# Kernel optimization log

Hardware: AMD Instinct MI355X
Metric: run time of the kernel (lower is better)

The kernel has to match this reference:

```python
import math
import jax, jax.numpy as jnp
import numpy as np

B_, L_, D_, N_, R_ = 4, 1024, 1024, 16, 64  # batch, seq, n_embd(=dim_inner), d_state, dt_rank


def setup_inputs() -> dict:
    key = jax.random.key(0)
    ks = jax.random.split(key, 6)
    s = lambda k, shp: jax.random.normal(k, shp, jnp.float32) * 0.02
    return {
        "x": jax.random.normal(ks[0], (B_, L_, D_), jnp.float32),
        "ln1_w": jnp.ones((D_,), jnp.float32),
        "ln2_w": jnp.ones((D_,), jnp.float32),
        "W_dbc": s(ks[1], (R_ + 2 * N_, D_)),   # x -> [delta_lowrank, B, C]
        "W_dt": s(ks[2], (D_, R_)),              # dt_rank -> dim_inner
        "b_dt": jnp.zeros((D_,), jnp.float32),
        "A_log": jnp.log(jnp.broadcast_to(jnp.arange(1, N_ + 1, dtype=jnp.float32), (D_, N_))),
        "Dp": jnp.ones((D_,), jnp.float32),      # skip-connection D parameter
        "W_fc": s(ks[3], (4 * D_, D_)),
        "W_proj": s(ks[4], (D_, 4 * D_)),
    }


def _layernorm(x, w):
    mu = jnp.mean(x, -1, keepdims=True)
    xc = x - mu
    var = jnp.mean(xc * xc, -1, keepdims=True)
    return xc * jax.lax.rsqrt(var + 1e-5) * w


def _new_gelu(x):
    c = math.sqrt(2.0 / math.pi)
    return 0.5 * x * (1.0 + jnp.tanh(c * (x + 0.044715 * x * x * x)))


def _ssm(x, W_dbc, W_dt, b_dt, A_log, Dp):
    # x: (b, l, d) with d == dim_inner == n_embd
    dbc = jnp.einsum("bld,ed->ble", x, W_dbc)                # (b,l,R+2N)
    delta, Bm, Cm = jnp.split(dbc, [R_, R_ + N_], axis=-1)
    delta = jax.nn.softplus(jnp.einsum("blr,dr->bld", delta, W_dt) + b_dt)  # (b,l,d)
    A = -jnp.exp(A_log)                                       # (d,n)
    dA = jnp.exp(delta[..., None] * A)                        # (b,l,d,n) discretized A
    dBx = (delta * x)[..., None] * Bm[:, :, None, :]          # (b,l,d,n) discretized B*x

    # h_t = dA_t * h_{t-1} + dBx_t  -> parallel first-order linear scan
    def combine(e1, e2):
        a1, b1 = e1
        a2, b2 = e2
        return a2 * a1, a2 * b1 + b2

    _, hs = jax.lax.associative_scan(combine, (dA, dBx), axis=1)
    y = jnp.einsum("bldn,bln->bld", hs, Cm)
    return y + x * Dp


def reference(x, ln1_w, ln2_w, W_dbc, W_dt, b_dt, A_log, Dp, W_fc, W_proj):
    h = jax.nn.softplus(_layernorm(x, ln1_w))
    h = h + _ssm(h, W_dbc, W_dt, b_dt, A_log, Dp)
    m = _layernorm(h, ln2_w)
    m = _new_gelu(jnp.einsum("bld,fd->blf", m, W_fc))
    m = jnp.einsum("blf,df->bld", m, W_proj)
    return h + m
```

## Files before the change

### kernel.cpp

```cpp
#include <hip/hip_runtime.h>
#include <cstdint>
#include <cstddef>

typedef unsigned short u16;
typedef unsigned int u32;
typedef __attribute__((ext_vector_type(8))) short short8;
typedef __attribute__((ext_vector_type(4))) float floatx4;
typedef __attribute__((ext_vector_type(4))) u16 u16x4;

#define DEV static __device__ __forceinline__

DEV u16 f2b(float f){ u32 u = __float_as_uint(f); u32 r = u + 0x7fffu + ((u>>16)&1u); return (u16)(r>>16); }
DEV float softplusf(float z){ return fmaxf(z,0.f) + log1pf(__expf(-fabsf(z))); }
DEV float fast_tanhf(float u){ float e = __expf(2.f*u); return 1.f - 2.f/(e+1.f); }
DEV float geluf(float x){ float u = 0.7978845608028654f*(x + 0.044715f*x*x*x); return 0.5f*x*(1.f+fast_tanhf(u)); }

DEV void async_copy16(const void* gp, void* lp){
  __builtin_amdgcn_global_load_lds((const __attribute__((address_space(1))) u32*)gp,
                                   (__attribute__((address_space(3))) u32*)lp, 16, 0, 0);
}

__global__ __launch_bounds__(256)
void prep_weights(const float* __restrict__ Wdbc, const float* __restrict__ Wdt,
                  const float* __restrict__ Wfc, const float* __restrict__ Wproj,
                  u16* __restrict__ dbc_b, u16* __restrict__ dt_b,
                  u16* __restrict__ fc_b, u16* __restrict__ pj_b)
{
  int i = blockIdx.x*256 + threadIdx.x;
  const float* src; u16* dst; int j;
  if (i < 32768){
    int e = i*4, r = e >> 10;
    if (r >= 96){ u16x4 z = {0,0,0,0}; *(u16x4*)(dbc_b + e) = z; return; }
    src = Wdbc; dst = dbc_b; j = i;
  } else if (i < 49152){ src = Wdt;   dst = dt_b; j = i - 32768; }
  else if (i < 1097728){ src = Wfc;   dst = fc_b; j = i - 49152; }
  else                 { src = Wproj; dst = pj_b; j = i - 1097728; }
  float4 v = ((const float4*)src)[j];
  u16x4 o = { f2b(v.x), f2b(v.y), f2b(v.z), f2b(v.w) };
  *(u16x4*)(dst + j*4) = o;
}

__global__ void dbc_post(const float* __restrict__ p, u16* __restrict__ delta_in,
                         float* __restrict__ BCf){
  int e = blockIdx.x*256 + threadIdx.x;
  int t = e >> 7, c = e & 127;
  float s = 0.f;
  #pragma unroll
  for (int z=0;z<8;z++) s += p[(size_t)z*524288 + e];
  if (c < 64)      delta_in[t*64 + c] = f2b(s);
  else if (c < 96) BCf[t*32 + (c-64)] = s;
}

__global__ void proj_reduce(const float* __restrict__ p, const float* __restrict__ h1f,
                            float* __restrict__ out){
  int i = blockIdx.x*256 + threadIdx.x;
  float4 a = ((const float4*)p)[i];
  float4 b = ((const float4*)(p + (size_t) 4194304))[i];
  float4 c = ((const float4*)(p + (size_t) 8388608))[i];
  float4 d = ((const float4*)(p + (size_t)12582912))[i];
  float4 r = ((const float4*)h1f)[i];
  float4 o = make_float4(a.x+b.x+c.x+d.x+r.x, a.y+b.y+c.y+d.y+r.y,
                         a.z+b.z+c.z+d.z+r.z, a.w+b.w+c.w+d.w+r.w);
  ((float4*)out)[i] = o;
}

__global__ __launch_bounds__(256)
void ln1_kernel(const float* __restrict__ x, const float* __restrict__ w,
                float* __restrict__ h0f, u16* __restrict__ h0b)
{
  int row = blockIdx.x, tid = threadIdx.x;
  const float4* xr = (const float4*)(x + (size_t)row*1024);
  float4 v = xr[tid];
  float s1 = v.x+v.y+v.z+v.w;
  float s2 = v.x*v.x+v.y*v.y+v.z*v.z+v.w*v.w;
  #pragma unroll
  for (int m=1;m<64;m<<=1){ s1 += __shfl_xor(s1,m); s2 += __shfl_xor(s2,m); }
  __shared__ float red[8];
  int wv = tid>>6;
  if ((tid&63)==0){ red[wv]=s1; red[4+wv]=s2; }
  __syncthreads();
  s1 = red[0]+red[1]+red[2]+red[3];
  s2 = red[4]+red[5]+red[6]+red[7];
  float mu  = s1*(1.f/1024.f);
  float var = s2*(1.f/1024.f) - mu*mu;
  float rstd = rsqrtf(var + 1e-5f);
  float4 wv4 = ((const float4*)w)[tid];
  float o0 = softplusf((v.x-mu)*rstd*wv4.x);
  float o1 = softplusf((v.y-mu)*rstd*wv4.y);
  float o2 = softplusf((v.z-mu)*rstd*wv4.z);
  float o3 = softplusf((v.w-mu)*rstd*wv4.w);
  ((float4*)(h0f + (size_t)row*1024))[tid] = make_float4(o0,o1,o2,o3);
  u16x4 ob = { f2b(o0), f2b(o1), f2b(o2), f2b(o3) };
  *(u16x4*)(h0b + (size_t)row*1024 + tid*4) = ob;
}

__global__ __launch_bounds__(256)
void ln2_kernel(const float* __restrict__ x, const float* __restrict__ w,
                u16* __restrict__ outb)
{
  int row = blockIdx.x, tid = threadIdx.x;
  const float4* xr = (const float4*)(x + (size_t)row*1024);
  float4 v = xr[tid];
  float s1 = v.x+v.y+v.z+v.w;
  float s2 = v.x*v.x+v.y*v.y+v.z*v.z+v.w*v.w;
  #pragma unroll
  for (int m=1;m<64;m<<=1){ s1 += __shfl_xor(s1,m); s2 += __shfl_xor(s2,m); }
  __shared__ float red[8];
  int wv = tid>>6;
  if ((tid&63)==0){ red[wv]=s1; red[4+wv]=s2; }
  __syncthreads();
  s1 = red[0]+red[1]+red[2]+red[3];
  s2 = red[4]+red[5]+red[6]+red[7];
  float mu  = s1*(1.f/1024.f);
  float var = s2*(1.f/1024.f) - mu*mu;
  float rstd = rsqrtf(var + 1e-5f);
  float4 wv4 = ((const float4*)w)[tid];
  u16x4 ob = { f2b((v.x-mu)*rstd*wv4.x), f2b((v.y-mu)*rstd*wv4.y),
               f2b((v.z-mu)*rstd*wv4.z), f2b((v.w-mu)*rstd*wv4.w) };
  *(u16x4*)(outb + (size_t)row*1024 + tid*4) = ob;
}

template<int EPI, int SWZ>
__global__ __launch_bounds__(256)
void gemm_bt(const u16* __restrict__ A, int lda,
             const u16* __restrict__ B, int ldb, int K,
             float* __restrict__ outF, u16* __restrict__ outB, int ldo,
             const float* __restrict__ bias, size_t zstr)
{
  __shared__ u16 sA[128*32];
  __shared__ u16 sB[128*32];
  const int tid = threadIdx.x;
  int m_blk, n_blk, zb;
  if (SWZ == 0){ n_blk = blockIdx.x; m_blk = blockIdx.y; zb = blockIdx.z; }
  else if (SWZ == 1){
    int b = blockIdx.x, xcd = b & 7, local = b >> 3;
    m_blk = (xcd>>2)*16 + (local & 15);
    n_blk = (xcd&3)*8 + (local >> 4);
    zb = 0;
  } else {
    int b = blockIdx.x, xcd = b & 7, local = b >> 3;
    m_blk = (xcd>>1)*8 + (local & 7);
    n_blk = local >> 3;
    zb = xcd & 1;
  }
  const int m0 = m_blk*128, n0 = n_blk*128;
  const int kstart = zb * K;
  const int wave = tid>>6, lane = tid&63;
  const int wm = (wave>>1)*64, wn = (wave&1)*64;
  const int lr = lane&15, quad = lane>>4;

  floatx4 acc[4][4];
  #pragma unroll
  for (int i=0;i<4;i++)
    #pragma unroll
    for (int j=0;j<4;j++){ floatx4 z = {0.f,0.f,0.f,0.f}; acc[i][j]=z; }

  const int r0 = tid>>2;
  const int kc8 = (((tid&3) ^ ((tid>>3)&3)))*8;
  const int sswz = ((lr>>1)&3);
  for (int k0=kstart; k0<kstart+K; k0+=32){
    __syncthreads();
    async_copy16(A + (size_t)(m0+r0)*lda    + k0+kc8, &sA[(size_t)tid*8]);
    async_copy16(A + (size_t)(m0+64+r0)*lda + k0+kc8, &sA[(size_t)(tid+256)*8]);
    async_copy16(B + (size_t)(n0+r0)*ldb    + k0+kc8, &sB[(size_t)tid*8]);
    async_copy16(B + (size_t)(n0+64+r0)*ldb + k0+kc8, &sB[(size_t)(tid+256)*8]);
    __syncthreads();
    short8 af[4], bf[4];
    #pragma unroll
    for (int i=0;i<4;i++){
      af[i] = *(const short8*)&sA[(wm+i*16+lr)*32 + (quad^sswz)*8];
      bf[i] = *(const short8*)&sB[(wn+i*16+lr)*32 + (quad^sswz)*8];
    }
    #pragma unroll
    for (int i=0;i<4;i++)
      #pragma unroll
      for (int j=0;j<4;j++)
        acc[i][j] = __builtin_amdgcn_mfma_f32_16x16x32_bf16(af[i], bf[j], acc[i][j], 0,0,0);
  }
  #pragma unroll
  for (int i=0;i<4;i++){
    #pragma unroll
    for (int j=0;j<4;j++){
      #pragma unroll
      for (int r=0;r<4;r++){
        int gr = m0 + wm + i*16 + quad*4 + r;
        int gc = n0 + wn + j*16 + lr;
        float v = acc[i][j][r];
        size_t o = (size_t)gr*ldo + gc;
        if (EPI==1)      outF[o] = softplusf(v + bias[gc]);
        else if (EPI==2) outB[o] = f2b(geluf(v));
        else             outF[zstr*zb + o] = v;
      }
    }
  }
}

template<int EPI, int SWZ>
__global__ __launch_bounds__(512, 2)
void gemm256(const u16* __restrict__ A, int lda,
             const u16* __restrict__ B, int ldb, int K,
             float* __restrict__ outF, u16* __restrict__ outB, int ldo,
             size_t zstr)
{
  __shared__ u16 sA[2][4][4096];
  __shared__ u16 sB[2][4][4096];
  const int tid = threadIdx.x;
  int m_blk, n_blk, zb;
  if (SWZ == 3){
    int b = blockIdx.x, xcd = b & 7, local = b >> 3;
    m_blk = (xcd>>2)*8 + (local & 7);
    n_blk = (xcd&3)*4 + (local >> 3);
    zb = 0;
  } else {
    int b = blockIdx.x, xcd = b & 7, local = b >> 3;
    zb    = xcd >> 1;
    m_blk = (xcd&1)*8 + (local & 7);
    n_blk = local >> 3;
  }
  const int m0 = m_blk*256, n0 = n_blk*256;
  const int kstart = zb*K;
  const int wave = tid>>6, lane = tid&63;
  const int mq = wave>>2, nq = wave&3;
  const int lr = lane&15, quad = lane>>4;
  const int sswz = (lr>>1)&3;

  const int srow = tid>>2;
  const int scol = ((tid&3) ^ ((tid>>3)&3))*8;
  const u16* pa = A + (size_t)(m0 + srow)*lda + scol;
  const u16* pb = B + (size_t)(n0 + srow)*ldb + scol;
  u16* la = (u16*)sA + tid*8;
  u16* lb = (u16*)sB + tid*8;
  const size_t ah128 = (size_t)128*lda;
  const size_t bh128 = (size_t)128*ldb;

  const int a_rd = (mq*64 + lr)*32 + (quad^sswz)*8;
  const int b_rd = ((nq&1)*64 + lr)*32 + (quad^sswz)*8;
  const int bun  = nq>>1;

  floatx4 acc[2][4][4];
  #pragma unroll
  for (int h=0;h<2;h++)
    #pragma unroll
    for (int i=0;i<4;i++)
      #pragma unroll
      for (int j=0;j<4;j++){ floatx4 z={0.f,0.f,0.f,0.f}; acc[h][i][j]=z; }

#define STG_A(NB,KS,H,KT) async_copy16(pa + (size_t)(H)*ah128 + (size_t)((KT) + (KS)*32), \
                                       la + (NB)*16384 + ((KS)*2+(H))*4096)
#define STG_B(NB,KS,H,KT) async_copy16(pb + (size_t)(H)*bh128 + (size_t)((KT) + (KS)*32), \
                                       lb + (NB)*16384 + ((KS)*2+(H))*4096)

#define PHASE(CUR, KA, AH, VM, ...)                                           \
  {                                                                           \
    asm volatile("s_waitcnt vmcnt(" VM ")" ::: "memory");                     \
    asm volatile("s_barrier" ::: "memory");                                   \
    __VA_ARGS__;                                                              \
    const u16* ca = (const u16*)sA + (CUR)*16384 + ((KA)*2+(AH))*4096;        \
    const u16* cb = (const u16*)sB + (CUR)*16384 + ((KA)*2+bun)*4096;         \
    short8 af[4], bf[4];                                                      \
    _Pragma("unroll")                                                         \
    for (int i_=0;i_<4;i_++){                                                 \
      af[i_] = *(const short8*)(ca + a_rd + i_*512);                          \
      bf[i_] = *(const short8*)(cb + b_rd + i_*512);                          \
    }                                                                         \
    __builtin_amdgcn_s_setprio(1);                                            \
    _Pragma("unroll")                                                         \
    for (int i_=0;i_<4;i_++)                                                  \
      _Pragma("unroll")                                                       \
      for (int j_=0;j_<4;j_++)                                                \
        acc[AH][i_][j_] = __builtin_amdgcn_mfma_f32_16x16x32_bf16(            \
            af[i_], bf[j_], acc[AH][i_][j_], 0,0,0);                          \
    __builtin_amdgcn_s_setprio(0);                                            \
  }

  STG_A(0,0,0,kstart); STG_B(0,0,0,kstart);
  STG_B(0,0,1,kstart); STG_A(0,0,1,kstart);
  STG_B(0,1,0,kstart); STG_B(0,1,1,kstart);
  STG_A(0,1,0,kstart); STG_A(0,1,1,kstart);

  const int NT = K >> 6;
  int cur = 0;
  int ktn = kstart + 64;
  for (int t=0; t<NT-1; ++t, ktn += 64, cur ^= 1){
    const int nb = cur^1;
    PHASE(cur, 0,0, "5", STG_A(nb,0,0,ktn); STG_B(nb,0,0,ktn));
    PHASE(cur, 0,1, "6", STG_B(nb,0,1,ktn); STG_A(nb,0,1,ktn));
    PHASE(cur, 1,0, "5", STG_B(nb,1,0,ktn); STG_B(nb,1,1,ktn));
    PHASE(cur, 1,1, "6", STG_A(nb,1,0,ktn); STG_A(nb,1,1,ktn));
  }
  PHASE(cur, 0,0, "5", );
  PHASE(cur, 0,1, "4", );
  PHASE(cur, 1,0, "1", );
  PHASE(cur, 1,1, "0", );

#undef PHASE
#undef STG_A
#undef STG_B

  #pragma unroll
  for (int h=0;h<2;h++){
    #pragma unroll
    for (int i=0;i<4;i++){
      #pragma unroll
      for (int j=0;j<4;j++){
        #pragma unroll
        for (int r=0;r<4;r++){
          int gr = m0 + h*128 + mq*64 + i*16 + quad*4 + r;
          int gc = n0 + nq*64 + j*16 + lr;
          float v = acc[h][i][j][r];
          size_t o = (size_t)gr*ldo + gc;
          if (EPI==2) outB[o] = f2b(geluf(v));
          else        outF[zstr*zb + o] = v;
        }
      }
    }
  }
}

__global__ __launch_bounds__(256)
void scan_p1(const float* __restrict__ delta, const float* __restrict__ h0f,
             const float* __restrict__ BCf, const float* __restrict__ A_log,
             float* __restrict__ Pbuf, float* __restrict__ Sbuf)
{
  int blk = blockIdx.x;
  int d = (blk & 3)*256 + threadIdx.x;
  int c = (blk >> 2) & 31;
  int b = blk >> 7;
  float a2[16], h[16], P[16];
  #pragma unroll
  for (int n=0;n<16;n++){ a2[n] = -__expf(A_log[d*16+n]) * 1.44269504f; h[n]=0.f; P[n]=1.f; }
  int t0 = c*32;
  const float* dptr = delta + ((size_t)(b*1024 + t0))*1024 + d;
  const float* xptr = h0f   + ((size_t)(b*1024 + t0))*1024 + d;
  const float* bc   = BCf   + ((size_t)(b*1024 + t0))*32;
  #pragma unroll 4
  for (int t=0;t<32;t++){
    float dlt = dptr[t*1024];
    float xv  = xptr[t*1024];
    float dx = dlt*xv;
    #pragma unroll
    for (int n=0;n<16;n++){
      float dA = exp2f(dlt*a2[n]);
      h[n] = dA*h[n] + dx*bc[t*32+n];
      P[n] *= dA;
    }
  }
  size_t base = ((size_t)((b*32 + c)*16))*1024 + d;
  #pragma unroll
  for (int n=0;n<16;n++){ Pbuf[base + (size_t)n*1024] = P[n]; Sbuf[base + (size_t)n*1024] = h[n]; }
}

__global__ __launch_bounds__(256)
void scan_p2(const float* __restrict__ Pbuf, const float* __restrict__ Sbuf,
             float* __restrict__ Hbuf)
{
  int blk = blockIdx.x;
  int d = (blk & 3)*256 + threadIdx.x;
  int n = (blk >> 2) & 15;
  int b = blk >> 6;
  float H = 0.f;
  for (int c=0;c<32;c++){
    size_t idx = ((size_t)((b*32 + c)*16 + n))*1024 + d;
    float P = Pbuf[idx], S = Sbuf[idx];
    Hbuf[idx] = H;
    H = P*H + S;
  }
}

__global__ __launch_bounds__(256)
void scan_p3(const float* __restrict__ delta, const float* __restrict__ h0f,
             const float* __restrict__ BCf, const float* __restrict__ A_log,
             const float* __restrict__ Hbuf, const float* __restrict__ Dp,
             float* __restrict__ h1f)
{
  int blk = blockIdx.x;
  int d = (blk & 3)*256 + threadIdx.x;
  int c = (blk >> 2) & 31;
  int b = blk >> 7;
  float a2[16], h[16];
  size_t hb = ((size_t)((b*32 + c)*16))*1024 + d;
  #pragma unroll
  for (int n=0;n<16;n++){
    a2[n] = -__expf(A_log[d*16+n]) * 1.44269504f;
    h[n] = Hbuf[hb + (size_t)n*1024];
  }
  float dpv = 1.f + Dp[d];
  int t0 = c*32;
  const float* dptr = delta + ((size_t)(b*1024 + t0))*1024 + d;
  const float* xptr = h0f   + ((size_t)(b*1024 + t0))*1024 + d;
  const float* bc   = BCf   + ((size_t)(b*1024 + t0))*32;
  float* optr = h1f + ((size_t)(b*1024 + t0))*1024 + d;
  #pragma unroll 4
  for (int t=0;t<32;t++){
    float dlt = dptr[t*1024];
    float xv  = xptr[t*1024];
    float dx = dlt*xv;
    float y = 0.f;
    #pragma unroll
    for (int n=0;n<16;n++){
      float dA = exp2f(dlt*a2[n]);
      h[n] = dA*h[n] + dx*bc[t*32+n];
      y += h[n]*bc[t*32+16+n];
    }
    optr[t*1024] = xv*dpv + y;
  }
}

extern "C" void kernel_launch(void* const* d_in, const int* in_sizes, int n_in,
                              void* d_out, int out_size, void* d_ws, size_t ws_size,
                              hipStream_t stream)
{
  const float* x    = (const float*)d_in[0];
  const float* ln1w = (const float*)d_in[1];
  const float* ln2w = (const float*)d_in[2];
  const float* Wdbc = (const float*)d_in[3];
  const float* Wdt  = (const float*)d_in[4];
  const float* bdt  = (const float*)d_in[5];
  const float* Alog = (const float*)d_in[6];
  const float* Dp   = (const float*)d_in[7];
  const float* Wfc  = (const float*)d_in[8];
  const float* Wproj= (const float*)d_in[9];
  float* out = (float*)d_out;

  char* ws = (char*)d_ws;
  size_t off = 0;
  auto carve = [&](size_t bytes)->char*{ char* p = ws + off; off += (bytes + 255) & ~(size_t)255; return p; };
  const size_t T = 4096;
  float* h0f   = (float*)carve(T*1024*4);
  float* h1f   = (float*)carve(T*1024*4);
  float* dlt   = (float*)carve(T*1024*4);
  float* Pbuf  = (float*)carve((size_t)4*32*16*1024*4);
  float* Sbuf  = (float*)carve((size_t)4*32*16*1024*4);
  float* Hbuf  = (float*)carve((size_t)4*32*16*1024*4);
  float* pad_  = (float*)carve((size_t)4*32*16*1024*4);
  float* BCf   = (float*)carve(T*32*4);
  u16*   h0b   = (u16*)  carve(T*1024*2);
  u16*   m0b   = (u16*)  carve(T*1024*2);
  u16*   g_b   = (u16*)  carve(T*4096*2);
  u16*   din_b = (u16*)  carve(T*64*2);
  u16*   Wdbc_b= (u16*)  carve((size_t)128*1024*2);
  u16*   Wdt_b = (u16*)  carve((size_t)1024*64*2);
  u16*   Wfc_b = (u16*)  carve((size_t)4096*1024*2);
  u16*   Wpj_b = (u16*)  carve((size_t)1024*4096*2);
  float* dbc_p  = Hbuf;
  float* proj_p = dlt;
  (void)pad_; (void)ws_size; (void)in_sizes; (void)n_in; (void)out_size;

  prep_weights<<<8384, 256, 0, stream>>>(Wdbc, Wdt, Wfc, Wproj,
                                         Wdbc_b, Wdt_b, Wfc_b, Wpj_b);

  ln1_kernel<<<4096, 256, 0, stream>>>(x, ln1w, h0f, h0b);

  gemm_bt<4,0><<<dim3(1,32,8), 256, 0, stream>>>(h0b, 1024, Wdbc_b, 1024, 128,
                                                 dbc_p, nullptr, 128, nullptr, (size_t)T*128);
  dbc_post<<<2048, 256, 0, stream>>>(dbc_p, din_b, BCf);

  gemm_bt<1,0><<<dim3(8,32), 256, 0, stream>>>(din_b, 64, Wdt_b, 64, 64,
                                               dlt, nullptr, 1024, bdt, 0);

  scan_p1<<<512, 256, 0, stream>>>(dlt, h0f, BCf, Alog, Pbuf, Sbuf);
  scan_p2<<<256, 256, 0, stream>>>(Pbuf, Sbuf, Hbuf);
  scan_p3<<<512, 256, 0, stream>>>(dlt, h0f, BCf, Alog, Hbuf, Dp, h1f);

  ln2_kernel<<<4096, 256, 0, stream>>>(h1f, ln2w, m0b);

  gemm256<2,3><<<256, 512, 0, stream>>>(m0b, 1024, Wfc_b, 1024, 1024,
                                        nullptr, g_b, 4096, 0);

  gemm256<4,4><<<256, 512, 0, stream>>>(g_b, 4096, Wpj_b, 4096, 1024,
                                        proj_p, nullptr, 1024, (size_t)T*1024);
  proj_reduce<<<4096, 256, 0, stream>>>(proj_p, h1f, out);
}
```

Measured before the change: 356.0 us.

## Restructure GEMM main-loop phases to overlap LDS reads with async loads

The K-loop phase is reordered. Each phase now reads its LDS fragments first, then issues the next async global->LDS copies, does a barrier and an lgkmcnt wait, runs the MFMAs, and only after that waits on vmcnt and barriers again. B fragments are loaded only once per K-slice and reused across both A halves, which cuts LDS reads. The epilogue is folded into the loop, with the last iteration issuing dummy loads from kstart so the vmcnt counts stay uniform. The cost is extra barriers and wasted global loads in the final iteration.

```diff
diff --git a/kernel.cpp b/kernel.cpp
--- a/kernel.cpp
+++ b/kernel.cpp
@@ -245,24 +245,27 @@
       #pragma unroll
       for (int j=0;j<4;j++){ floatx4 z={0.f,0.f,0.f,0.f}; acc[h][i][j]=z; }
 
+  short8 af[4], bf[4];
+
 #define STG_A(NB,KS,H,KT) async_copy16(pa + (size_t)(H)*ah128 + (size_t)((KT) + (KS)*32), \
                                        la + (NB)*16384 + ((KS)*2+(H))*4096)
 #define STG_B(NB,KS,H,KT) async_copy16(pb + (size_t)(H)*bh128 + (size_t)((KT) + (KS)*32), \
                                        lb + (NB)*16384 + ((KS)*2+(H))*4096)
 
-#define PHASE(CUR, KA, AH, VM, ...)                                           \
+#define PHASE(CUR, KS, AH, VM, ...)                                           \
   {                                                                           \
-    asm volatile("s_waitcnt vmcnt(" VM ")" ::: "memory");                     \
-    asm volatile("s_barrier" ::: "memory");                                   \
+    const u16* ca = (const u16*)sA + (CUR)*16384 + ((KS)*2+(AH))*4096;        \
+    _Pragma("unroll")                                                         \
+    for (int i_=0;i_<4;i_++) af[i_] = *(const short8*)(ca + a_rd + i_*512);   \
+    if ((AH)==0){                                                             \
+      const u16* cb = (const u16*)sB + (CUR)*16384 + ((KS)*2+bun)*4096;       \
+      _Pragma("unroll")                                                       \
+      for (int i_=0;i_<4;i_++) bf[i_] = *(const short8*)(cb + b_rd + i_*512); \
+    }                                                                         \
     __VA_ARGS__;                                                              \
-    const u16* ca = (const u16*)sA + (CUR)*16384 + ((KA)*2+(AH))*4096;        \
-    const u16* cb = (const u16*)sB + (CUR)*16384 + ((KA)*2+bun)*4096;         \
-    short8 af[4], bf[4];                                                      \
-    _Pragma("unroll")                                                         \
-    for (int i_=0;i_<4;i_++){                                                 \
-      af[i_] = *(const short8*)(ca + a_rd + i_*512);                          \
-      bf[i_] = *(const short8*)(cb + b_rd + i_*512);                          \
-    }                                                                         \
+    __builtin_amdgcn_s_barrier();                                             \
+    asm volatile("s_waitcnt lgkmcnt(0)" ::: "memory");                        \
+    __builtin_amdgcn_sched_barrier(0);                                        \
     __builtin_amdgcn_s_setprio(1);                                            \
     _Pragma("unroll")                                                         \
     for (int i_=0;i_<4;i_++)                                                  \
@@ -271,27 +274,28 @@
         acc[AH][i_][j_] = __builtin_amdgcn_mfma_f32_16x16x32_bf16(            \
             af[i_], bf[j_], acc[AH][i_][j_], 0,0,0);                          \
     __builtin_amdgcn_s_setprio(0);                                            \
+    asm volatile("s_waitcnt vmcnt(" VM ")" ::: "memory");                     \
+    __builtin_amdgcn_s_barrier();                                             \
   }
 
   STG_A(0,0,0,kstart); STG_B(0,0,0,kstart);
   STG_B(0,0,1,kstart); STG_A(0,0,1,kstart);
   STG_B(0,1,0,kstart); STG_B(0,1,1,kstart);
   STG_A(0,1,0,kstart); STG_A(0,1,1,kstart);
+  asm volatile("s_waitcnt vmcnt(5)" ::: "memory");
+  __builtin_amdgcn_s_barrier();
 
   const int NT = K >> 6;
   int cur = 0;
   int ktn = kstart + 64;
-  for (int t=0; t<NT-1; ++t, ktn += 64, cur ^= 1){
+  for (int t=0; t<NT; ++t, ktn += 64, cur ^= 1){
     const int nb = cur^1;
-    PHASE(cur, 0,0, "5", STG_A(nb,0,0,ktn); STG_B(nb,0,0,ktn));
-    PHASE(cur, 0,1, "6", STG_B(nb,0,1,ktn); STG_A(nb,0,1,ktn));
-    PHASE(cur, 1,0, "5", STG_B(nb,1,0,ktn); STG_B(nb,1,1,ktn));
-    PHASE(cur, 1,1, "6", STG_A(nb,1,0,ktn); STG_A(nb,1,1,ktn));
-  }
-  PHASE(cur, 0,0, "5", );
-  PHASE(cur, 0,1, "4", );
-  PHASE(cur, 1,0, "1", );
-  PHASE(cur, 1,1, "0", );
+    const int kt = (t < NT-1) ? ktn : kstart;
+    PHASE(cur, 0,0, "6", STG_A(nb,0,0,kt); STG_B(nb,0,0,kt));
+    PHASE(cur, 0,1, "5", STG_B(nb,0,1,kt); STG_A(nb,0,1,kt));
+    PHASE(cur, 1,0, "6", STG_B(nb,1,0,kt); STG_B(nb,1,1,kt));
+    PHASE(cur, 1,1, "5", STG_A(nb,1,0,kt); STG_A(nb,1,1,kt));
+  }
 
 #undef PHASE
 #undef STG_A
```

After: 333.9 us. 6.2% less time.
